# Kernel optimization log

Measured on AMD Instinct MI355X. Metric: run time of the kernel, lower is better.

The kernel has to match this reference:

```python
import jax, jax.numpy as jnp
import numpy as np

NUM_CLASSES = 10  # CINIC-10


def setup_inputs() -> dict:
    key = jax.random.key(0)
    k1, k2 = jax.random.split(key)
    embeddings = jax.random.normal(k1, (131072, 512), dtype=jnp.float32)
    labels = jax.random.randint(k2, (131072,), 0, NUM_CLASSES)
    return {"embeddings": embeddings, "labels": labels}


def reference(embeddings, labels):
    # Per-class mean (prototypes) as a segment reduction. With all classes
    # present, torch.unique(labels) == [0..9] sorted, so the remapped
    # target_indices equal labels directly.
    n = embeddings.shape[0]
    sums = jax.ops.segment_sum(embeddings, labels, num_segments=NUM_CLASSES)  # [C, d]
    counts = jax.ops.segment_sum(jnp.ones((n,), embeddings.dtype), labels,
                                 num_segments=NUM_CLASSES)                    # [C]
    prototypes = sums / counts[:, None]

    # Squared Euclidean distances: ||e||^2 + ||p||^2 - 2 e.p  (== cdist(...)**2)
    sq_e = jnp.sum(embeddings * embeddings, axis=1, keepdims=True)  # [B, 1]
    sq_p = jnp.sum(prototypes * prototypes, axis=1)                 # [C]
    d2 = sq_e + sq_p[None, :] - 2.0 * (embeddings @ prototypes.T)   # [B, C]
    d2 = jnp.maximum(d2, 0.0)

    logits = -d2
    logp = jax.nn.log_softmax(logits, axis=-1)
    loss = -jnp.mean(jnp.take_along_axis(logp, labels[:, None], axis=1))
    return (loss, logits)
```

## Files before the change

### kernel.cpp

```cpp
#include <hip/hip_runtime.h>

#define NROWS   131072
#define DIMS    512
#define NC      10
#define SEG_BLOCKS 1024
#define SUMSTRIDE 5120

typedef __attribute__((ext_vector_type(8))) short short8;
typedef __attribute__((ext_vector_type(4))) float floatx4;


static __device__ __forceinline__ unsigned int pk2(float lo, float hi) {
    return (__float_as_uint(hi) & 0xFFFF0000u) | (__float_as_uint(lo) >> 16);
}

static __device__ __forceinline__ short8 pack8(const float4 a, const float4 b) {
    union { unsigned int u[4]; short8 v; } r;
    r.u[0] = pk2(a.x, a.y);
    r.u[1] = pk2(a.z, a.w);
    r.u[2] = pk2(b.x, b.y);
    r.u[3] = pk2(b.z, b.w);
    return r.v;
}


__global__ __launch_bounds__(256) void k_seg(const float* __restrict__ E,
                                             const int* __restrict__ L,
                                             float* __restrict__ part,
                                             int* __restrict__ counts,
                                             uint2* __restrict__ E16,
                                             float* __restrict__ norms) {
    __shared__ float4 R[NC * 128];
    __shared__ float ns[4 * 64];
    __shared__ int lc[16];
    const int tid  = threadIdx.x;
    const int half = tid >> 7;
    const int dt   = tid & 127;
    const int wid  = tid >> 6;
    const int lane = tid & 63;
    if (tid < 16) lc[tid] = 0;
    __syncthreads();

    const int rows0 = blockIdx.x * 128;
    const float4* Ev = (const float4*)E;

    float4 z = {0.f, 0.f, 0.f, 0.f};
    float4 a0=z,a1=z,a2=z,a3=z,a4=z,a5=z,a6=z,a7=z,a8=z,a9=z;

    int idx = (rows0 + half) * 128 + dt;
    float4 v0 = Ev[idx];
    float4 v1 = Ev[idx + 256];
    int l0 = L[rows0 + half];
    int l1 = L[rows0 + 2 + half];

    for (int i = 0; i < 64; ++i) {
        float4 v2; int l2;
        const bool pf = (i < 62);
        if (pf) {
            v2 = Ev[idx + 512];
            l2 = L[rows0 + 2 * i + 4 + half];
        }
        if (dt == 0) atomicAdd(&lc[l0], 1);

        uint2 uu;
        uu.x = pk2(v0.x, v0.y);
        uu.y = pk2(v0.z, v0.w);
        E16[idx] = uu;

        float p = v0.x*v0.x + v0.y*v0.y + v0.z*v0.z + v0.w*v0.w;
        p += __shfl_xor(p, 1);  p += __shfl_xor(p, 2);
        p += __shfl_xor(p, 4);  p += __shfl_xor(p, 8);
        p += __shfl_xor(p, 16); p += __shfl_xor(p, 32);
        if (lane == 0) ns[wid * 64 + i] = p;

        switch (l0) {
            case 0: a0.x+=v0.x; a0.y+=v0.y; a0.z+=v0.z; a0.w+=v0.w; break;
            case 1: a1.x+=v0.x; a1.y+=v0.y; a1.z+=v0.z; a1.w+=v0.w; break;
            case 2: a2.x+=v0.x; a2.y+=v0.y; a2.z+=v0.z; a2.w+=v0.w; break;
            case 3: a3.x+=v0.x; a3.y+=v0.y; a3.z+=v0.z; a3.w+=v0.w; break;
            case 4: a4.x+=v0.x; a4.y+=v0.y; a4.z+=v0.z; a4.w+=v0.w; break;
            case 5: a5.x+=v0.x; a5.y+=v0.y; a5.z+=v0.z; a5.w+=v0.w; break;
            case 6: a6.x+=v0.x; a6.y+=v0.y; a6.z+=v0.z; a6.w+=v0.w; break;
            case 7: a7.x+=v0.x; a7.y+=v0.y; a7.z+=v0.z; a7.w+=v0.w; break;
            case 8: a8.x+=v0.x; a8.y+=v0.y; a8.z+=v0.z; a8.w+=v0.w; break;
            default: a9.x+=v0.x; a9.y+=v0.y; a9.z+=v0.z; a9.w+=v0.w; break;
        }
        v0 = v1; l0 = l1;
        if (pf) { v1 = v2; l1 = l2; }
        idx += 256;
    }

    if (half) {
        R[0*128+dt]=a0; R[1*128+dt]=a1; R[2*128+dt]=a2; R[3*128+dt]=a3;
        R[4*128+dt]=a4; R[5*128+dt]=a5; R[6*128+dt]=a6; R[7*128+dt]=a7;
        R[8*128+dt]=a8; R[9*128+dt]=a9;
    }
    __syncthreads();
    if (!half) {
        float4* dst = (float4*)(part + (size_t)blockIdx.x * SUMSTRIDE);
        float4 t;
#define MERGE_ST(c, ac)                                                       \
        t = R[(c)*128 + dt];                                                  \
        t.x += ac.x; t.y += ac.y; t.z += ac.z; t.w += ac.w;                   \
        dst[(c)*128 + dt] = t;
        MERGE_ST(0,a0) MERGE_ST(1,a1) MERGE_ST(2,a2) MERGE_ST(3,a3)
        MERGE_ST(4,a4) MERGE_ST(5,a5) MERGE_ST(6,a6) MERGE_ST(7,a7)
        MERGE_ST(8,a8) MERGE_ST(9,a9)
#undef MERGE_ST
    }
    if (tid < 128) {
        const int i2 = tid >> 1, h2 = tid & 1;
        norms[rows0 + tid] = ns[(2*h2)*64 + i2] + ns[(2*h2+1)*64 + i2];
    }
    if (tid < 16) counts[blockIdx.x * 16 + tid] = lc[tid];
}


__global__ __launch_bounds__(256) void k_red(const float* __restrict__ part,
                                             float* __restrict__ psum8) {
    __shared__ float m[128];
    const int t   = threadIdx.x;
    const int col = t & 127, kh = t >> 7;
    const int cc  = blockIdx.x % 40;
    const int kc  = blockIdx.x / 40;
    const int e   = cc * 128 + col;

    const float* base = part + (size_t)(kc * 128 + kh * 64) * SUMSTRIDE + e;
    float s0=0.f, s1=0.f, s2=0.f, s3=0.f;
    for (int j = 0; j < 64; j += 4) {
        s0 += base[(size_t)(j + 0) * SUMSTRIDE];
        s1 += base[(size_t)(j + 1) * SUMSTRIDE];
        s2 += base[(size_t)(j + 2) * SUMSTRIDE];
        s3 += base[(size_t)(j + 3) * SUMSTRIDE];
    }
    float s = (s0 + s1) + (s2 + s3);
    if (kh) m[col] = s;
    __syncthreads();
    if (!kh) psum8[kc * SUMSTRIDE + e] = s + m[col];
}


__global__ __launch_bounds__(512) void k_pp(const float* __restrict__ psum8,
                                            const int* __restrict__ counts,
                                            float* __restrict__ p2,
                                            float* __restrict__ pn,
                                            float* __restrict__ out) {
    __shared__ float P[16 * DIMS];
    __shared__ int tmp[512];
    __shared__ int cnt[16];
    const int t = threadIdx.x;

    {
        const int c0 = t & 15, chunk = t >> 4;
        int s = 0;
        for (int j = 0; j < 32; ++j) s += counts[(chunk * 32 + j) * 16 + c0];
        tmp[t] = s;
    }
    __syncthreads();
    if (t < 16) {
        int n = 0;
        for (int ch = 0; ch < 32; ++ch) n += tmp[ch * 16 + t];
        cnt[t] = n;
    }
    if (t == 0) out[0] = 0.f;
    __syncthreads();

    for (int e = t; e < 16 * DIMS; e += 512) {
        const int c = e >> 9;
        float val = 0.f;
        if (c < NC) {
            float s = 0.f;
#pragma unroll
            for (int j = 0; j < 8; ++j) s += psum8[j * SUMSTRIDE + e];
            val = 2.f * s / (float)cnt[c];
        }
        p2[e] = val;
        P[e] = val;
    }
    __syncthreads();

    const int w = t >> 6, lane = t & 63;
    const float4* Pv = (const float4*)P;
    for (int sdx = 0; sdx < 2; ++sdx) {
        const int c = w + sdx * 8;
        float4 a = Pv[c * 128 + lane * 2];
        float4 b = Pv[c * 128 + lane * 2 + 1];
        float ss = a.x*a.x + a.y*a.y + a.z*a.z + a.w*a.w
                 + b.x*b.x + b.y*b.y + b.z*b.z + b.w*b.w;
        ss += __shfl_xor(ss, 1);  ss += __shfl_xor(ss, 2);
        ss += __shfl_xor(ss, 4);  ss += __shfl_xor(ss, 8);
        ss += __shfl_xor(ss, 16); ss += __shfl_xor(ss, 32);
        if (lane == 0) pn[c] = 0.25f * ss;
    }
}


__global__ __launch_bounds__(256, 2) void k_main(const ushort* __restrict__ E16,
                                                 const float* __restrict__ norms,
                                                 const int* __restrict__ L,
                                                 const float* __restrict__ p2,
                                                 const float* __restrict__ pn,
                                                 float* __restrict__ out) {
    const int tid  = threadIdx.x;
    const int wid  = tid >> 6, lane = tid & 63;
    const int c16  = lane & 15, quad = lane >> 4;

    short8 bf[16];
    const float4* P = (const float4*)p2;
#pragma unroll
    for (int kt = 0; kt < 16; ++kt) {
        float4 a = P[c16 * 128 + kt * 8 + quad * 2];
        float4 b = P[c16 * 128 + kt * 8 + quad * 2 + 1];
        bf[kt] = pack8(a, b);
    }
    const float pnc = pn[c16];

    float lossp = 0.f;
    const int gw = blockIdx.x * 4 + wid;
    for (int t = gw; t < 8192; t += 4096) {
        const int tile  = 8191 - t;
        const int rbase = tile * 16;
        const short8* A = (const short8*)(E16 + (size_t)(rbase + c16) * DIMS);
        const float nmine = norms[rbase + c16];

        floatx4 acc = {0.f, 0.f, 0.f, 0.f};
#pragma unroll
        for (int kt = 0; kt < 16; ++kt) {
            acc = __builtin_amdgcn_mfma_f32_16x16x32_bf16(A[kt * 4 + quad],
                                                          bf[kt], acc, 0, 0, 0);
        }

#pragma unroll
        for (int i = 0; i < 4; ++i) {
            const int row = rbase + quad * 4 + i;
            const float nr = __shfl(nmine, quad * 4 + i);
            float lg = acc[i] - nr - pnc;
            lg = fminf(lg, 0.f);
            float ml = (c16 < NC) ? lg : -3.0e38f;
            ml = fmaxf(ml, __shfl_xor(ml, 1));
            ml = fmaxf(ml, __shfl_xor(ml, 2));
            ml = fmaxf(ml, __shfl_xor(ml, 4));
            ml = fmaxf(ml, __shfl_xor(ml, 8));
            float ex = (c16 < NC) ? __expf(lg - ml) : 0.f;
            ex += __shfl_xor(ex, 1);
            ex += __shfl_xor(ex, 2);
            ex += __shfl_xor(ex, 4);
            ex += __shfl_xor(ex, 8);
            const float lse = ml + __logf(ex);
            if (c16 < NC) out[1 + row * NC + c16] = lg;
            const int lab = L[row];
            if (c16 == lab) lossp += lse - lg;
        }
    }

    lossp += __shfl_xor(lossp, 1);  lossp += __shfl_xor(lossp, 2);
    lossp += __shfl_xor(lossp, 4);  lossp += __shfl_xor(lossp, 8);
    lossp += __shfl_xor(lossp, 16); lossp += __shfl_xor(lossp, 32);
    __shared__ float ls[4];
    if (lane == 0) ls[wid] = lossp;
    __syncthreads();
    if (tid == 0)
        atomicAdd(out, (ls[0] + ls[1] + ls[2] + ls[3]) * (1.0f / (float)NROWS));
}


extern "C" void kernel_launch(void* const* d_in, const int* in_sizes, int n_in,
                              void* d_out, int out_size, void* d_ws, size_t ws_size,
                              hipStream_t stream) {
    const float* E = (const float*)d_in[0];
    const int*   L = (const int*)d_in[1];
    float* out = (float*)d_out;
    char* ws = (char*)d_ws;

    float* part   = (float*)ws;
    float* psum8  = (float*)(ws + 20971520);
    int*   counts = (int*)  (ws + 21135360);
    float* p2     = (float*)(ws + 21200896);
    float* pn     = (float*)(ws + 21233664);
    float* norms  = (float*)(ws + 21233728);
    uint2* E16    = (uint2*)(ws + 21758016);

    k_seg <<<SEG_BLOCKS, 256, 0, stream>>>(E, L, part, counts, E16, norms);
    k_red <<<320,        256, 0, stream>>>(part, psum8);
    k_pp  <<<1,          512, 0, stream>>>(psum8, counts, p2, pn, out);
    k_main<<<1024,       256, 0, stream>>>((const ushort*)E16, norms, L, p2, pn, out);
}
```

Measured before the change: 453.1 us.

## Drop bf16 staging copy, read fp32 in main kernel, merge reduction kernels

The segment kernel no longer writes a bf16 copy of the embeddings. The main kernel now reads the fp32 embeddings directly and packs them to bf16 in registers before each MFMA. The two-stage partial-sum reduction and the single-block prototype kernel are merged into one 64-block kernel that also computes the class counts. Prototype norms are now computed inside the main kernel. This removes a 128 MB bf16 write and one launch, but the main kernel reads twice as many bytes and the reduction now runs on only 40 active blocks, each doing a long serial 512-row loop.

```diff
diff --git a/kernel.cpp b/kernel.cpp
--- a/kernel.cpp
+++ b/kernel.cpp
@@ -28,7 +28,6 @@
                                              const int* __restrict__ L,
                                              float* __restrict__ part,
                                              int* __restrict__ counts,
-                                             uint2* __restrict__ E16,
                                              float* __restrict__ norms) {
     __shared__ float4 R[NC * 128];
     __shared__ float ns[4 * 64];
@@ -61,11 +60,6 @@
             l2 = L[rows0 + 2 * i + 4 + half];
         }
         if (dt == 0) atomicAdd(&lc[l0], 1);
-
-        uint2 uu;
-        uu.x = pk2(v0.x, v0.y);
-        uu.y = pk2(v0.z, v0.w);
-        E16[idx] = uu;
 
         float p = v0.x*v0.x + v0.y*v0.y + v0.z*v0.z + v0.w*v0.w;
         p += __shfl_xor(p, 1);  p += __shfl_xor(p, 2);
@@ -116,18 +110,41 @@
 }
 
 
-__global__ __launch_bounds__(256) void k_red(const float* __restrict__ part,
-                                             float* __restrict__ psum8) {
+__global__ __launch_bounds__(256) void k_red2(const float* __restrict__ part,
+                                              const int* __restrict__ counts,
+                                              float* __restrict__ p2,
+                                              float* __restrict__ out) {
     __shared__ float m[128];
-    const int t   = threadIdx.x;
+    __shared__ int cs[256];
+    const int t = threadIdx.x;
+    const int b = blockIdx.x;
     const int col = t & 127, kh = t >> 7;
-    const int cc  = blockIdx.x % 40;
-    const int kc  = blockIdx.x / 40;
-    const int e   = cc * 128 + col;
-
-    const float* base = part + (size_t)(kc * 128 + kh * 64) * SUMSTRIDE + e;
+
+    if (b >= 40) {
+        if (kh == 0) p2[5120 + (b - 40) * 128 + col] = 0.f;
+        return;
+    }
+    if (b == 0 && t == 0) out[0] = 0.f;
+
+    const int c = b >> 2;
+    {
+        int s = 0;
+        for (int j = t; j < 1024; j += 256) s += counts[j * 16 + c];
+        cs[t] = s;
+    }
+    __syncthreads();
+    if (t < 64) cs[t] += cs[t + 64] + cs[t + 128] + cs[t + 192];
+    __syncthreads();
+    if (t < 8)  cs[t] += cs[t + 8] + cs[t + 16] + cs[t + 24] + cs[t + 32]
+                       + cs[t + 40] + cs[t + 48] + cs[t + 56];
+    __syncthreads();
+    if (t == 0) cs[0] += cs[1] + cs[2] + cs[3] + cs[4] + cs[5] + cs[6] + cs[7];
+    __syncthreads();
+    const float inv = 1.f / (float)cs[0];
+
+    const float* base = part + (size_t)(kh * 512) * SUMSTRIDE + b * 128 + col;
     float s0=0.f, s1=0.f, s2=0.f, s3=0.f;
-    for (int j = 0; j < 64; j += 4) {
+    for (int j = 0; j < 512; j += 4) {
         s0 += base[(size_t)(j + 0) * SUMSTRIDE];
         s1 += base[(size_t)(j + 1) * SUMSTRIDE];
         s2 += base[(size_t)(j + 2) * SUMSTRIDE];
@@ -136,98 +153,49 @@
     float s = (s0 + s1) + (s2 + s3);
     if (kh) m[col] = s;
     __syncthreads();
-    if (!kh) psum8[kc * SUMSTRIDE + e] = s + m[col];
-}
-
-
-__global__ __launch_bounds__(512) void k_pp(const float* __restrict__ psum8,
-                                            const int* __restrict__ counts,
-                                            float* __restrict__ p2,
-                                            float* __restrict__ pn,
-                                            float* __restrict__ out) {
-    __shared__ float P[16 * DIMS];
-    __shared__ int tmp[512];
-    __shared__ int cnt[16];
-    const int t = threadIdx.x;
-
-    {
-        const int c0 = t & 15, chunk = t >> 4;
-        int s = 0;
-        for (int j = 0; j < 32; ++j) s += counts[(chunk * 32 + j) * 16 + c0];
-        tmp[t] = s;
-    }
-    __syncthreads();
-    if (t < 16) {
-        int n = 0;
-        for (int ch = 0; ch < 32; ++ch) n += tmp[ch * 16 + t];
-        cnt[t] = n;
-    }
-    if (t == 0) out[0] = 0.f;
-    __syncthreads();
-
-    for (int e = t; e < 16 * DIMS; e += 512) {
-        const int c = e >> 9;
-        float val = 0.f;
-        if (c < NC) {
-            float s = 0.f;
-#pragma unroll
-            for (int j = 0; j < 8; ++j) s += psum8[j * SUMSTRIDE + e];
-            val = 2.f * s / (float)cnt[c];
-        }
-        p2[e] = val;
-        P[e] = val;
-    }
-    __syncthreads();
-
-    const int w = t >> 6, lane = t & 63;
-    const float4* Pv = (const float4*)P;
-    for (int sdx = 0; sdx < 2; ++sdx) {
-        const int c = w + sdx * 8;
-        float4 a = Pv[c * 128 + lane * 2];
-        float4 b = Pv[c * 128 + lane * 2 + 1];
-        float ss = a.x*a.x + a.y*a.y + a.z*a.z + a.w*a.w
-                 + b.x*b.x + b.y*b.y + b.z*b.z + b.w*b.w;
-        ss += __shfl_xor(ss, 1);  ss += __shfl_xor(ss, 2);
-        ss += __shfl_xor(ss, 4);  ss += __shfl_xor(ss, 8);
-        ss += __shfl_xor(ss, 16); ss += __shfl_xor(ss, 32);
-        if (lane == 0) pn[c] = 0.25f * ss;
-    }
-}
-
-
-__global__ __launch_bounds__(256, 2) void k_main(const ushort* __restrict__ E16,
+    if (!kh) p2[b * 128 + col] = 2.f * (s + m[col]) * inv;
+}
+
+
+__global__ __launch_bounds__(256, 2) void k_main(const float* __restrict__ E,
                                                  const float* __restrict__ norms,
                                                  const int* __restrict__ L,
                                                  const float* __restrict__ p2,
-                                                 const float* __restrict__ pn,
                                                  float* __restrict__ out) {
     const int tid  = threadIdx.x;
     const int wid  = tid >> 6, lane = tid & 63;
     const int c16  = lane & 15, quad = lane >> 4;
 
     short8 bf[16];
+    float ss = 0.f;
     const float4* P = (const float4*)p2;
 #pragma unroll
     for (int kt = 0; kt < 16; ++kt) {
         float4 a = P[c16 * 128 + kt * 8 + quad * 2];
         float4 b = P[c16 * 128 + kt * 8 + quad * 2 + 1];
+        ss += a.x*a.x + a.y*a.y + a.z*a.z + a.w*a.w
+            + b.x*b.x + b.y*b.y + b.z*b.z + b.w*b.w;
         bf[kt] = pack8(a, b);
     }
-    const float pnc = pn[c16];
+    ss += __shfl_xor(ss, 16);
+    ss += __shfl_xor(ss, 32);
+    const float pnc = 0.25f * ss;
 
     float lossp = 0.f;
     const int gw = blockIdx.x * 4 + wid;
     for (int t = gw; t < 8192; t += 4096) {
         const int tile  = 8191 - t;
         const int rbase = tile * 16;
-        const short8* A = (const short8*)(E16 + (size_t)(rbase + c16) * DIMS);
+        const float4* A = (const float4*)(E + (size_t)(rbase + c16) * DIMS);
         const float nmine = norms[rbase + c16];
 
         floatx4 acc = {0.f, 0.f, 0.f, 0.f};
 #pragma unroll
         for (int kt = 0; kt < 16; ++kt) {
-            acc = __builtin_amdgcn_mfma_f32_16x16x32_bf16(A[kt * 4 + quad],
-                                                          bf[kt], acc, 0, 0, 0);
+            float4 a = A[kt * 8 + quad * 2];
+            float4 b = A[kt * 8 + quad * 2 + 1];
+            acc = __builtin_amdgcn_mfma_f32_16x16x32_bf16(pack8(a, b), bf[kt],
+                                                          acc, 0, 0, 0);
         }
 
 #pragma unroll
@@ -273,15 +241,11 @@
     char* ws = (char*)d_ws;
 
     float* part   = (float*)ws;
-    float* psum8  = (float*)(ws + 20971520);
-    int*   counts = (int*)  (ws + 21135360);
-    float* p2     = (float*)(ws + 21200896);
-    float* pn     = (float*)(ws + 21233664);
-    float* norms  = (float*)(ws + 21233728);
-    uint2* E16    = (uint2*)(ws + 21758016);
-
-    k_seg <<<SEG_BLOCKS, 256, 0, stream>>>(E, L, part, counts, E16, norms);
-    k_red <<<320,        256, 0, stream>>>(part, psum8);
-    k_pp  <<<1,          512, 0, stream>>>(psum8, counts, p2, pn, out);
-    k_main<<<1024,       256, 0, stream>>>((const ushort*)E16, norms, L, p2, pn, out);
-}
+    int*   counts = (int*)  (ws + 20971520);
+    float* p2     = (float*)(ws + 21037056);
+    float* norms  = (float*)(ws + 21069824);
+
+    k_seg <<<SEG_BLOCKS, 256, 0, stream>>>(E, L, part, counts, norms);
+    k_red2<<<64,         256, 0, stream>>>(part, counts, p2, out);
+    k_main<<<1024,       256, 0, stream>>>(E, norms, L, p2, out);
+}
```

Measured after the change: 499.7 us. 1.1x slower.
